# Kernel tuning notes

Measured on AMD Instinct MI355X. Metric: run time of the kernel, lower is better.

## Reference

```python
import jax, jax.numpy as jnp
import numpy as np

NUM_GRAPHS = 64
NODE_SZ = 200
FEAT = 200
HID = 256          # hidden_size; each signed branch outputs HID//2
HALF = HID // 2
N_NODES = NUM_GRAPHS * NODE_SZ
N_EDGES = 409600
NUM_LAYERS = 3


def _lin_init(key, out_f, in_f):
    kw, kb = jax.random.split(key)
    s = 1.0 / np.sqrt(in_f)
    W = jax.random.uniform(kw, (out_f, in_f), minval=-s, maxval=s, dtype=jnp.float32)
    b = jax.random.uniform(kb, (out_f,), minval=-s, maxval=s, dtype=jnp.float32)
    return W, b


def setup_inputs() -> dict:
    key = jax.random.key(0)
    ks = jax.random.split(key, 16)
    x = jax.random.normal(ks[0], (N_NODES, FEAT), dtype=jnp.float32)
    edge_index = jax.random.randint(ks[1], (2, N_EDGES), 0, N_NODES, dtype=jnp.int64)
    edge_weight = jax.random.normal(ks[2], (N_EDGES,), dtype=jnp.float32)
    batch = jnp.repeat(jnp.arange(NUM_GRAPHS, dtype=jnp.int64), NODE_SZ)

    # signed conv layer params: layer0 in=FEAT, layers 1..: in=HID; each lin maps 2*in -> HALF
    Wp0, bp0 = _lin_init(ks[3], HALF, 2 * FEAT)
    Wn0, bn0 = _lin_init(ks[4], HALF, 2 * FEAT)
    Wp1, bp1 = _lin_init(ks[5], HALF, 2 * HID)
    Wn1, bn1 = _lin_init(ks[6], HALF, 2 * HID)
    Wp2, bp2 = _lin_init(ks[7], HALF, 2 * HID)
    Wn2, bn2 = _lin_init(ks[8], HALF, 2 * HID)
    Wr, br = _lin_init(ks[9], HID, NODE_SZ * HID)   # readout_lin
    Wl, bl = _lin_init(ks[10], 1, HID)              # final lin
    return dict(x=x, edge_index=edge_index, edge_weight=edge_weight, batch=batch,
                Wp0=Wp0, bp0=bp0, Wn0=Wn0, bn0=bn0,
                Wp1=Wp1, bp1=bp1, Wn1=Wn1, bn1=bn1,
                Wp2=Wp2, bp2=bp2, Wn2=Wn2, bn2=bn2,
                Wr=Wr, br=br, Wl=Wl, bl=bl)


def _signed_conv(x, src, dst, w, Wp, bp, Wn, bn):
    # edge-weighted signed mean aggregation, split by weight sign
    xs = x[src]                                   # [E, D] gather
    pw = jnp.where(w > 0, w, 0.0)
    nw = jnp.where(w < 0, -w, 0.0)
    agg_p = jax.ops.segment_sum(pw[:, None] * xs, dst, num_segments=N_NODES)
    agg_n = jax.ops.segment_sum(nw[:, None] * xs, dst, num_segments=N_NODES)
    deg_p = jax.ops.segment_sum((w > 0).astype(x.dtype), dst, num_segments=N_NODES)
    deg_n = jax.ops.segment_sum((w < 0).astype(x.dtype), dst, num_segments=N_NODES)
    agg_p = agg_p / jnp.maximum(deg_p, 1.0)[:, None]
    agg_n = agg_n / jnp.maximum(deg_n, 1.0)[:, None]
    hp = jnp.concatenate([agg_p, x], -1) @ Wp.T + bp
    hn = jnp.concatenate([agg_n, x], -1) @ Wn.T + bn
    return jnp.concatenate([hp, hn], -1)          # [N, HID]


def reference(x, edge_index, edge_weight, batch,
              Wp0, bp0, Wn0, bn0, Wp1, bp1, Wn1, bn1, Wp2, bp2, Wn2, bn2,
              Wr, br, Wl, bl):
    src, dst = edge_index[0], edge_index[1]
    convs = [(Wp0, bp0, Wn0, bn0), (Wp1, bp1, Wn1, bn1), (Wp2, bp2, Wn2, bn2)]
    h = x
    for i, (Wp, bp, Wn, bn) in enumerate(convs):
        h = _signed_conv(h, src, dst, edge_weight, Wp, bp, Wn, bn)
        if i < NUM_LAYERS - 1:
            h = jax.nn.leaky_relu(h, negative_slope=0.01)
    # per-graph readout: batch is contiguous with NODE_SZ nodes per graph,
    # so the boolean-mask+view loop is exactly a reshape.
    g = h.reshape(NUM_GRAPHS, NODE_SZ * HID)
    g = g @ Wr.T + br                             # [G, HID]
    # dropout(p=0.5) is identity in eval mode
    return g @ Wl.T + bl                          # [G, 1]
```

## Files before the change

### kernel.cpp

```cpp
#include <hip/hip_runtime.h>

#define NUM_GRAPHS 64
#define NODE_SZ    200
#define FEAT       200
#define HID        256
#define HALF       128
#define N_NODES    (NUM_GRAPHS * NODE_SZ)
#define KREAD      (NODE_SZ * HID)
#define KSTRIDE    512
#define HBLK       128

typedef unsigned short ushort_t;
typedef unsigned int uint_t;
typedef __attribute__((ext_vector_type(8))) short bf16x8;
typedef __attribute__((ext_vector_type(4))) float f32x4;

#define GAS(p) ((const __attribute__((address_space(1))) void*)(p))
#define LAS(p) ((__attribute__((address_space(3))) void*)(p))

__device__ __forceinline__ float bf2f(ushort_t u) {
    union { unsigned int i; float f; } v; v.i = ((unsigned int)u) << 16; return v.f;
}
__device__ __forceinline__ ushort_t f2bf(float f) {
    union { float f; unsigned int i; } v; v.f = f;
    unsigned int x = v.i;
    unsigned int r = (x + 0x7fffu + ((x >> 16) & 1u)) >> 16;
    return (ushort_t)r;
}

__global__ __launch_bounds__(1024) void bhist_kernel(const int* __restrict__ ei,
                                                     const float* __restrict__ ew,
                                                     uint_t* __restrict__ bh, int E) {
    __shared__ uint_t h[N_NODES];
    for (int i = threadIdx.x; i < N_NODES; i += 1024) h[i] = 0;
    __syncthreads();
    int b = blockIdx.x;
    int epb = (E + HBLK - 1) / HBLK;
    int e0 = b * epb, e1 = min(e0 + epb, E);
    for (int e = e0 + threadIdx.x; e < e1; e += 1024) {
        int dst = ei[E + e];
        float w = ew[e];
        if (w > 0.0f)      atomicAdd(&h[dst], 1u);
        else if (w < 0.0f) atomicAdd(&h[dst], 0x10000u);
    }
    __syncthreads();
    uint_t* out = bh + (size_t)b * N_NODES;
    for (int i = threadIdx.x * 4; i < N_NODES; i += 4096)
        *(uint4*)&out[i] = *(const uint4*)&h[i];
}

__global__ void colpref_kernel(uint_t* __restrict__ bh, int* __restrict__ counts,
                               int* __restrict__ cnt_p) {
    int n = blockIdx.x * 256 + threadIdx.x;
    if (n >= N_NODES) return;
    uint_t seq = 0;
    for (int b = 0; b < HBLK; ++b) {
        size_t i = (size_t)b * N_NODES + n;
        uint_t v = bh[i];
        bh[i] = seq;
        seq += v;
    }
    counts[n] = (int)((seq & 0xffffu) + (seq >> 16));
    cnt_p[n]  = (int)(seq & 0xffffu);
}

__global__ __launch_bounds__(1024) void scan_kernel(const int* __restrict__ counts,
                                                    const int* __restrict__ cnt_p,
                                                    uint2* __restrict__ obnd, int n) {
    const int PER = 13;
    int t = threadIdx.x;
    int start = t * PER;
    int local[PER];
    int sum = 0;
#pragma unroll
    for (int i = 0; i < PER; ++i) {
        int idx = start + i;
        int v = (idx < n) ? counts[idx] : 0;
        local[i] = sum;
        sum += v;
    }
    int lane = t & 63, wid = t >> 6;
    int inc = sum;
#pragma unroll
    for (int d = 1; d < 64; d <<= 1) {
        int up = __shfl_up(inc, d);
        if (lane >= d) inc += up;
    }
    __shared__ int wsum[16], woff[16];
    if (lane == 63) wsum[wid] = inc;
    __syncthreads();
    if (t < 16) {
        int acc = 0;
        for (int j = 0; j < 16; ++j) if (j < t) acc += wsum[j];
        woff[t] = acc;
    }
    __syncthreads();
    int base = woff[wid] + (inc - sum);
#pragma unroll
    for (int i = 0; i < PER; ++i) {
        int idx = start + i;
        if (idx < n) {
            uint_t off = (uint_t)(base + local[i]);
            obnd[idx] = make_uint2(off, off + (uint_t)cnt_p[idx]);
        }
    }
    if (t == 1023) {
        uint_t tot = (uint_t)(base + sum);
        obnd[n] = make_uint2(tot, tot);
    }
}

__global__ __launch_bounds__(1024) void scat_kernel(const int* __restrict__ ei,
                                                    const float* __restrict__ ew,
                                                    const uint_t* __restrict__ bh,
                                                    const uint2* __restrict__ obnd,
                                                    uint2* __restrict__ es, int E) {
    __shared__ uint_t cur[N_NODES];
    int b = blockIdx.x;
    const uint_t* pref = bh + (size_t)b * N_NODES;
    for (int i = threadIdx.x * 4; i < N_NODES; i += 4096)
        *(uint4*)&cur[i] = *(const uint4*)&pref[i];
    __syncthreads();
    int epb = (E + HBLK - 1) / HBLK;
    int e0 = b * epb, e1 = min(e0 + epb, E);
    for (int e = e0 + threadIdx.x; e < e1; e += 1024) {
        int src = ei[e];
        int dst = ei[E + e];
        float w = ew[e];
        if (w > 0.0f) {
            uint_t old = atomicAdd(&cur[dst], 1u);
            uint_t pos = obnd[dst].x + (old & 0xffffu);
            es[pos] = make_uint2((uint_t)src, __float_as_uint(w));
        } else if (w < 0.0f) {
            uint_t old = atomicAdd(&cur[dst], 0x10000u);
            uint_t pos = obnd[dst].y + (old >> 16);
            es[pos] = make_uint2((uint_t)src, __float_as_uint(-w));
        }
    }
}

__global__ void prep_kernel(const float* __restrict__ W0p, const float* __restrict__ W0n,
                            const float* __restrict__ W1p, const float* __restrict__ W1n,
                            const float* __restrict__ W2p, const float* __restrict__ W2n,
                            const float* __restrict__ x,
                            ushort_t* __restrict__ wcast, ushort_t* __restrict__ xb) {
    int task = blockIdx.y;
    if (task < 6) {
        if (blockIdx.x >= 256) return;
        const float* W = (task == 0) ? W0p : (task == 1) ? W0n : (task == 2) ? W1p
                       : (task == 3) ? W1n : (task == 4) ? W2p : W2n;
        int K2 = (task < 2) ? 400 : 512;
        int idx = blockIdx.x * 256 + threadIdx.x;
        int row = idx >> 9;
        int col = idx & (KSTRIDE - 1);
        wcast[task * 65536 + idx] = (col < K2) ? f2bf(W[(size_t)row * K2 + col]) : (ushort_t)0;
    } else {
        int i = (blockIdx.x * 256 + threadIdx.x) * 4;
        if (i >= N_NODES * FEAT) return;
        float4 v = *(const float4*)&x[i];
        ushort4 o;
        o.x = f2bf(v.x); o.y = f2bf(v.y); o.z = f2bf(v.z); o.w = f2bf(v.w);
        *(ushort4*)&xb[i] = o;
    }
}

template <int D>
__global__ __launch_bounds__(256) void agg_kernel(
        const ushort_t* __restrict__ hb,
        const uint2* __restrict__ obnd,
        const uint2* __restrict__ es,
        ushort_t* __restrict__ Ap, ushort_t* __restrict__ An) {
    constexpr int ACT = D / 4;
    int lane = threadIdx.x & 63;
    int wv   = threadIdx.x >> 6;
    int n = blockIdx.x * 4 + wv;
    int c0 = min(lane, ACT - 1) * 4;
    uint2 ob = obnd[n];
    uint_t off = ob.x, mid = ob.y, end = obnd[n + 1].x;

    float ap[4] = {0.f, 0.f, 0.f, 0.f};
    float an[4] = {0.f, 0.f, 0.f, 0.f};

#pragma unroll 1
    for (int phase = 0; phase < 2; ++phase) {
        uint_t lo = phase ? mid : off;
        uint_t hi = phase ? end : mid;
        float* acc = phase ? an : ap;
#pragma unroll 1
        for (uint_t base = lo; base < hi; base += 64) {
            int cnt = (int)min(64u, hi - base);
            uint2 rec = es[base + (uint_t)min(lane, cnt - 1)];
            int i = 0;
#pragma unroll 1
            for (; i + 8 <= cnt; i += 8) {
                int s[8]; float w[8]; uint2 p[8];
#pragma unroll
                for (int j = 0; j < 8; ++j) {
                    s[j] = __shfl((int)rec.x, i + j);
                    w[j] = __uint_as_float((uint_t)__shfl((int)rec.y, i + j));
                }
#pragma unroll
                for (int j = 0; j < 8; ++j) p[j] = *(const uint2*)&hb[(size_t)s[j] * D + c0];
#pragma unroll
                for (int j = 0; j < 8; ++j) {
                    const ushort_t* q = (const ushort_t*)&p[j];
#pragma unroll
                    for (int c = 0; c < 4; ++c) acc[c] = fmaf(w[j], bf2f(q[c]), acc[c]);
                }
            }
#pragma unroll 1
            for (; i < cnt; ++i) {
                int s = __shfl((int)rec.x, i);
                float w = __uint_as_float((uint_t)__shfl((int)rec.y, i));
                uint2 pk = *(const uint2*)&hb[(size_t)s * D + c0];
                const ushort_t* q = (const ushort_t*)&pk;
#pragma unroll
                for (int c = 0; c < 4; ++c) acc[c] = fmaf(w, bf2f(q[c]), acc[c]);
            }
        }
    }

    size_t rb = (size_t)n * KSTRIDE;
    if (lane < ACT) {
        float dp = fmaxf((float)(mid - off), 1.0f);
        float dn = fmaxf((float)(end - mid), 1.0f);
        uint2 pk = *(const uint2*)&hb[(size_t)n * D + c0];
        const ushort_t* p = (const ushort_t*)&pk;
        ushort4 os = {p[0], p[1], p[2], p[3]};
        ushort4 op, on;
        op.x = f2bf(ap[0] / dp); op.y = f2bf(ap[1] / dp);
        op.z = f2bf(ap[2] / dp); op.w = f2bf(ap[3] / dp);
        on.x = f2bf(an[0] / dn); on.y = f2bf(an[1] / dn);
        on.z = f2bf(an[2] / dn); on.w = f2bf(an[3] / dn);
        *(ushort4*)&Ap[rb + c0] = op;
        *(ushort4*)&An[rb + c0] = on;
        *(ushort4*)&Ap[rb + D + c0] = os;
        *(ushort4*)&An[rb + D + c0] = os;
    }
    if (D == 200 && lane >= 50 && lane < 54) {
        ushort4 z = {0, 0, 0, 0};
        *(ushort4*)&Ap[rb + 400 + (lane - 50) * 4] = z;
        *(ushort4*)&An[rb + 400 + (lane - 50) * 4] = z;
    }
}

template <int KSTEPS, bool LEAKY>
__global__ __launch_bounds__(256) void conv_mfma(
        const ushort_t* __restrict__ Ap, const ushort_t* __restrict__ An,
        const ushort_t* __restrict__ Wpb, const ushort_t* __restrict__ Wnb,
        const float* __restrict__ bp, const float* __restrict__ bn,
        ushort_t* __restrict__ hout) {
    __shared__ __align__(16) ushort_t As[2][64 * 32];
    __shared__ __align__(16) ushort_t Bs[2][128 * 32];
    int mBase = blockIdx.x * 64;
    bool neg = (blockIdx.y != 0);
    const ushort_t* A    = neg ? An : Ap;
    const ushort_t* W    = neg ? Wnb : Wpb;
    const float*    bias = neg ? bn : bp;
    int tid  = threadIdx.x;
    int lane = tid & 63;
    int wv   = tid >> 6;
    int r    = lane & 15;
    int quad = lane >> 4;

    int rowA = tid >> 2, colA = (tid & 3) * 8;
    const ushort_t* gA  = A + (size_t)(mBase + rowA) * KSTRIDE + colA;
    const ushort_t* gB0 = W + (size_t)rowA * KSTRIDE + colA;
    const ushort_t* gB1 = W + (size_t)(rowA + 64) * KSTRIDE + colA;

    f32x4 acc[8];
#pragma unroll
    for (int j = 0; j < 8; ++j) acc[j] = (f32x4){0.f, 0.f, 0.f, 0.f};

    __builtin_amdgcn_global_load_lds(GAS(gA),  LAS(&As[0][wv * 512]), 16, 0, 0);
    __builtin_amdgcn_global_load_lds(GAS(gB0), LAS(&Bs[0][wv * 512]), 16, 0, 0);
    __builtin_amdgcn_global_load_lds(GAS(gB1), LAS(&Bs[0][2048 + wv * 512]), 16, 0, 0);

    for (int kt = 0; kt < KSTEPS; ++kt) {
        int cur = kt & 1;
        __syncthreads();
        if (kt + 1 < KSTEPS) {
            int kB = (kt + 1) * 32;
            __builtin_amdgcn_global_load_lds(GAS(gA + kB),  LAS(&As[cur ^ 1][wv * 512]), 16, 0, 0);
            __builtin_amdgcn_global_load_lds(GAS(gB0 + kB), LAS(&Bs[cur ^ 1][wv * 512]), 16, 0, 0);
            __builtin_amdgcn_global_load_lds(GAS(gB1 + kB), LAS(&Bs[cur ^ 1][2048 + wv * 512]), 16, 0, 0);
        }
        bf16x8 a = *(const bf16x8*)&As[cur][(wv * 16 + r) * 32 + quad * 8];
#pragma unroll
        for (int j = 0; j < 8; ++j) {
            bf16x8 b = *(const bf16x8*)&Bs[cur][(j * 16 + r) * 32 + quad * 8];
            acc[j] = __builtin_amdgcn_mfma_f32_16x16x32_bf16(a, b, acc[j], 0, 0, 0);
        }
    }
    int colOff = neg ? HALF : 0;
#pragma unroll
    for (int j = 0; j < 8; ++j) {
        int c = j * 16 + r;
        float bv = bias[c];
#pragma unroll
        for (int reg = 0; reg < 4; ++reg) {
            int m = mBase + wv * 16 + quad * 4 + reg;
            float v = acc[j][reg] + bv;
            if (LEAKY) v = (v > 0.0f) ? v : 0.01f * v;
            hout[(size_t)m * HID + colOff + c] = f2bf(v);
        }
    }
}

__global__ __launch_bounds__(256) void readout_mfma(
        const ushort_t* __restrict__ h, const float* __restrict__ Wr,
        float* __restrict__ g_ws) {
    __shared__ __align__(16) ushort_t As[64 * 32];
    __shared__ __align__(16) ushort_t Bs[64 * 32];
    int nBase  = blockIdx.x * 64;
    int kStart = blockIdx.y * 800;
    int tid  = threadIdx.x;
    int lane = tid & 63;
    int wv   = tid >> 6;
    int r    = lane & 15;
    int quad = lane >> 4;

    f32x4 acc[4];
#pragma unroll
    for (int j = 0; j < 4; ++j) acc[j] = (f32x4){0.f, 0.f, 0.f, 0.f};

    for (int kt = 0; kt < 25; ++kt) {
        int kBase = kStart + kt * 32;
        int lin = tid * 8;
        int row = lin >> 5, col = lin & 31;
        *(uint4*)&As[lin] = *(const uint4*)&h[(size_t)row * KREAD + kBase + col];
        {
            const float* wp = &Wr[(size_t)(nBase + row) * KREAD + kBase + col];
            float4 f0 = *(const float4*)&wp[0];
            float4 f1 = *(const float4*)&wp[4];
            ushort4 b0, b1;
            b0.x = f2bf(f0.x); b0.y = f2bf(f0.y); b0.z = f2bf(f0.z); b0.w = f2bf(f0.w);
            b1.x = f2bf(f1.x); b1.y = f2bf(f1.y); b1.z = f2bf(f1.z); b1.w = f2bf(f1.w);
            *(ushort4*)&Bs[lin]     = b0;
            *(ushort4*)&Bs[lin + 4] = b1;
        }
        __syncthreads();
        bf16x8 a = *(const bf16x8*)&As[(wv * 16 + r) * 32 + quad * 8];
#pragma unroll
        for (int j = 0; j < 4; ++j) {
            bf16x8 b = *(const bf16x8*)&Bs[(j * 16 + r) * 32 + quad * 8];
            acc[j] = __builtin_amdgcn_mfma_f32_16x16x32_bf16(a, b, acc[j], 0, 0, 0);
        }
        __syncthreads();
    }
#pragma unroll
    for (int j = 0; j < 4; ++j) {
        int c = nBase + j * 16 + r;
#pragma unroll
        for (int reg = 0; reg < 4; ++reg) {
            int g = wv * 16 + quad * 4 + reg;
            atomicAdd(&g_ws[g * HID + c], acc[j][reg]);
        }
    }
}

__global__ void final_kernel(const float* __restrict__ g_ws, const float* __restrict__ br,
                             const float* __restrict__ Wl, const float* __restrict__ bl,
                             float* __restrict__ out) {
    int g = blockIdx.x;
    int c = threadIdx.x;
    float v = (g_ws[g * HID + c] + br[c]) * Wl[c];
#pragma unroll
    for (int d = 32; d > 0; d >>= 1) v += __shfl_down(v, d);
    __shared__ float s[4];
    if ((c & 63) == 0) s[c >> 6] = v;
    __syncthreads();
    if (c == 0) out[g] = s[0] + s[1] + s[2] + s[3] + bl[0];
}

extern "C" void kernel_launch(void* const* d_in, const int* in_sizes, int n_in,
                              void* d_out, int out_size, void* d_ws, size_t ws_size,
                              hipStream_t stream) {
    const float* x  = (const float*)d_in[0];
    const int*   ei = (const int*)d_in[1];
    const float* ew = (const float*)d_in[2];
    const float* Wp0 = (const float*)d_in[4];
    const float* bp0 = (const float*)d_in[5];
    const float* Wn0 = (const float*)d_in[6];
    const float* bn0 = (const float*)d_in[7];
    const float* Wp1 = (const float*)d_in[8];
    const float* bp1 = (const float*)d_in[9];
    const float* Wn1 = (const float*)d_in[10];
    const float* bn1 = (const float*)d_in[11];
    const float* Wp2 = (const float*)d_in[12];
    const float* bp2 = (const float*)d_in[13];
    const float* Wn2 = (const float*)d_in[14];
    const float* bn2 = (const float*)d_in[15];
    const float* Wr  = (const float*)d_in[16];
    const float* br  = (const float*)d_in[17];
    const float* Wl  = (const float*)d_in[18];
    const float* bl  = (const float*)d_in[19];
    const int E = in_sizes[1] / 2;

    char* ws = (char*)d_ws;
    float*    g_ws   = (float*)(ws + 0);
    uint_t*   bh     = (uint_t*)(ws + 65536);
    int*      counts = (int*)(ws + 6619136);
    int*      cnt_p  = (int*)(ws + 6670336);
    uint2*    obnd   = (uint2*)(ws + 6721536);
    uint2*    es     = (uint2*)(ws + 6824000);
    ushort_t* Ap     = (ushort_t*)(ws + 10100800);
    ushort_t* An     = (ushort_t*)(ws + 23208000);
    ushort_t* hA     = (ushort_t*)(ws + 36315200);
    ushort_t* hB     = (ushort_t*)(ws + 42868800);
    ushort_t* wcast  = (ushort_t*)(ws + 49422400);
    ushort_t* xb     = (ushort_t*)(ws + 50208832);

    ushort_t* w0p = wcast + 0 * 65536;
    ushort_t* w0n = wcast + 1 * 65536;
    ushort_t* w1p = wcast + 2 * 65536;
    ushort_t* w1n = wcast + 3 * 65536;
    ushort_t* w2p = wcast + 4 * 65536;
    ushort_t* w2n = wcast + 5 * 65536;

    hipMemsetAsync(g_ws, 0, 65536, stream);

    hipLaunchKernelGGL(bhist_kernel, dim3(HBLK), dim3(1024), 0, stream, ei, ew, bh, E);
    hipLaunchKernelGGL(colpref_kernel, dim3((N_NODES + 255) / 256), dim3(256), 0, stream,
                       bh, counts, cnt_p);
    hipLaunchKernelGGL(scan_kernel, dim3(1), dim3(1024), 0, stream, counts, cnt_p, obnd, N_NODES);
    hipLaunchKernelGGL(scat_kernel, dim3(HBLK), dim3(1024), 0, stream, ei, ew, bh, obnd, es, E);

    hipLaunchKernelGGL(prep_kernel, dim3(2500, 7), dim3(256), 0, stream,
                       Wp0, Wn0, Wp1, Wn1, Wp2, Wn2, x, wcast, xb);

    hipLaunchKernelGGL((agg_kernel<FEAT>), dim3(N_NODES / 4), dim3(256), 0, stream,
                       xb, obnd, es, Ap, An);
    hipLaunchKernelGGL((conv_mfma<13, true>), dim3(N_NODES / 64, 2), dim3(256), 0, stream,
                       Ap, An, w0p, w0n, bp0, bn0, hA);
    hipLaunchKernelGGL((agg_kernel<HID>), dim3(N_NODES / 4), dim3(256), 0, stream,
                       hA, obnd, es, Ap, An);
    hipLaunchKernelGGL((conv_mfma<16, true>), dim3(N_NODES / 64, 2), dim3(256), 0, stream,
                       Ap, An, w1p, w1n, bp1, bn1, hB);
    hipLaunchKernelGGL((agg_kernel<HID>), dim3(N_NODES / 4), dim3(256), 0, stream,
                       hB, obnd, es, Ap, An);
    hipLaunchKernelGGL((conv_mfma<16, false>), dim3(N_NODES / 64, 2), dim3(256), 0, stream,
                       Ap, An, w2p, w2n, bp2, bn2, hA);

    hipLaunchKernelGGL(readout_mfma, dim3(4, 64), dim3(256), 0, stream, hA, Wr, g_ws);
    hipLaunchKernelGGL(final_kernel, dim3(NUM_GRAPHS), dim3(256), 0, stream,
                       g_ws, br, Wl, bl, (float*)d_out);
}
```

Baseline: 315.2 us.

## Fuse signed aggregation with per-layer MFMA linear into one kernel

Each conv layer now runs as a single kernel: a 32-node block gathers the positive and negative neighbour sums into an LDS tile (padded stride) and immediately multiplies it by the branch weight via MFMA, writing the activated output. This removes the Ap/An global intermediate buffers (write plus re-read of about 13 MB per layer) and three kernel launches. In exchange, each block does 8 serial gathers per wave per branch before any MFMA work, with less parallelism (400 blocks) and no overlap between gather and matmul. The weight tiles are also reloaded per block.

Result: slower. 390.5 us (+23.9%).

```diff
diff --git a/kernel.cpp b/kernel.cpp
--- a/kernel.cpp
+++ b/kernel.cpp
@@ -8,6 +8,7 @@
 #define N_NODES    (NUM_GRAPHS * NODE_SZ)
 #define KREAD      (NODE_SZ * HID)
 #define KSTRIDE    512
+#define ASTRIDE    544
 #define HBLK       128
 
 typedef unsigned short ushort_t;
@@ -165,144 +166,144 @@
 }
 
 template <int D>
-__global__ __launch_bounds__(256) void agg_kernel(
+__device__ __forceinline__ void gather_bucket(const ushort_t* __restrict__ hb,
+                                              const uint2* __restrict__ es,
+                                              uint_t lo, uint_t hi, int c0, int lane,
+                                              float acc[4]) {
+#pragma unroll 1
+    for (uint_t base = lo; base < hi; base += 64) {
+        int cnt = (int)min(64u, hi - base);
+        uint2 rec = es[base + (uint_t)min(lane, cnt - 1)];
+        int i = 0;
+#pragma unroll 1
+        for (; i + 8 <= cnt; i += 8) {
+            int s[8]; float w[8]; uint2 p[8];
+#pragma unroll
+            for (int j = 0; j < 8; ++j) {
+                s[j] = __shfl((int)rec.x, i + j);
+                w[j] = __uint_as_float((uint_t)__shfl((int)rec.y, i + j));
+            }
+#pragma unroll
+            for (int j = 0; j < 8; ++j) p[j] = *(const uint2*)&hb[(size_t)s[j] * D + c0];
+#pragma unroll
+            for (int j = 0; j < 8; ++j) {
+                const ushort_t* q = (const ushort_t*)&p[j];
+#pragma unroll
+                for (int c = 0; c < 4; ++c) acc[c] = fmaf(w[j], bf2f(q[c]), acc[c]);
+            }
+        }
+#pragma unroll 1
+        for (; i < cnt; ++i) {
+            int s = __shfl((int)rec.x, i);
+            float w = __uint_as_float((uint_t)__shfl((int)rec.y, i));
+            uint2 pk = *(const uint2*)&hb[(size_t)s * D + c0];
+            const ushort_t* q = (const ushort_t*)&pk;
+#pragma unroll
+            for (int c = 0; c < 4; ++c) acc[c] = fmaf(w, bf2f(q[c]), acc[c]);
+        }
+    }
+}
+
+template <int D, int KSTEPS, bool LEAKY>
+__global__ __launch_bounds__(256) void fused_layer(
         const ushort_t* __restrict__ hb,
-        const uint2* __restrict__ obnd,
-        const uint2* __restrict__ es,
-        ushort_t* __restrict__ Ap, ushort_t* __restrict__ An) {
-    constexpr int ACT = D / 4;
-    int lane = threadIdx.x & 63;
-    int wv   = threadIdx.x >> 6;
-    int n = blockIdx.x * 4 + wv;
-    int c0 = min(lane, ACT - 1) * 4;
-    uint2 ob = obnd[n];
-    uint_t off = ob.x, mid = ob.y, end = obnd[n + 1].x;
-
-    float ap[4] = {0.f, 0.f, 0.f, 0.f};
-    float an[4] = {0.f, 0.f, 0.f, 0.f};
-
-#pragma unroll 1
-    for (int phase = 0; phase < 2; ++phase) {
-        uint_t lo = phase ? mid : off;
-        uint_t hi = phase ? end : mid;
-        float* acc = phase ? an : ap;
-#pragma unroll 1
-        for (uint_t base = lo; base < hi; base += 64) {
-            int cnt = (int)min(64u, hi - base);
-            uint2 rec = es[base + (uint_t)min(lane, cnt - 1)];
-            int i = 0;
-#pragma unroll 1
-            for (; i + 8 <= cnt; i += 8) {
-                int s[8]; float w[8]; uint2 p[8];
-#pragma unroll
-                for (int j = 0; j < 8; ++j) {
-                    s[j] = __shfl((int)rec.x, i + j);
-                    w[j] = __uint_as_float((uint_t)__shfl((int)rec.y, i + j));
-                }
-#pragma unroll
-                for (int j = 0; j < 8; ++j) p[j] = *(const uint2*)&hb[(size_t)s[j] * D + c0];
-#pragma unroll
-                for (int j = 0; j < 8; ++j) {
-                    const ushort_t* q = (const ushort_t*)&p[j];
-#pragma unroll
-                    for (int c = 0; c < 4; ++c) acc[c] = fmaf(w[j], bf2f(q[c]), acc[c]);
-                }
-            }
-#pragma unroll 1
-            for (; i < cnt; ++i) {
-                int s = __shfl((int)rec.x, i);
-                float w = __uint_as_float((uint_t)__shfl((int)rec.y, i));
-                uint2 pk = *(const uint2*)&hb[(size_t)s * D + c0];
-                const ushort_t* q = (const ushort_t*)&pk;
-#pragma unroll
-                for (int c = 0; c < 4; ++c) acc[c] = fmaf(w, bf2f(q[c]), acc[c]);
-            }
-        }
-    }
-
-    size_t rb = (size_t)n * KSTRIDE;
-    if (lane < ACT) {
-        float dp = fmaxf((float)(mid - off), 1.0f);
-        float dn = fmaxf((float)(end - mid), 1.0f);
-        uint2 pk = *(const uint2*)&hb[(size_t)n * D + c0];
-        const ushort_t* p = (const ushort_t*)&pk;
-        ushort4 os = {p[0], p[1], p[2], p[3]};
-        ushort4 op, on;
-        op.x = f2bf(ap[0] / dp); op.y = f2bf(ap[1] / dp);
-        op.z = f2bf(ap[2] / dp); op.w = f2bf(ap[3] / dp);
-        on.x = f2bf(an[0] / dn); on.y = f2bf(an[1] / dn);
-        on.z = f2bf(an[2] / dn); on.w = f2bf(an[3] / dn);
-        *(ushort4*)&Ap[rb + c0] = op;
-        *(ushort4*)&An[rb + c0] = on;
-        *(ushort4*)&Ap[rb + D + c0] = os;
-        *(ushort4*)&An[rb + D + c0] = os;
-    }
-    if (D == 200 && lane >= 50 && lane < 54) {
-        ushort4 z = {0, 0, 0, 0};
-        *(ushort4*)&Ap[rb + 400 + (lane - 50) * 4] = z;
-        *(ushort4*)&An[rb + 400 + (lane - 50) * 4] = z;
-    }
-}
-
-template <int KSTEPS, bool LEAKY>
-__global__ __launch_bounds__(256) void conv_mfma(
-        const ushort_t* __restrict__ Ap, const ushort_t* __restrict__ An,
+        const uint2* __restrict__ obnd, const uint2* __restrict__ es,
         const ushort_t* __restrict__ Wpb, const ushort_t* __restrict__ Wnb,
         const float* __restrict__ bp, const float* __restrict__ bn,
         ushort_t* __restrict__ hout) {
-    __shared__ __align__(16) ushort_t As[2][64 * 32];
+    __shared__ __align__(16) ushort_t At[32 * ASTRIDE];
     __shared__ __align__(16) ushort_t Bs[2][128 * 32];
-    int mBase = blockIdx.x * 64;
-    bool neg = (blockIdx.y != 0);
-    const ushort_t* A    = neg ? An : Ap;
-    const ushort_t* W    = neg ? Wnb : Wpb;
-    const float*    bias = neg ? bn : bp;
+    constexpr int ACT = D / 4;
     int tid  = threadIdx.x;
     int lane = tid & 63;
     int wv   = tid >> 6;
     int r    = lane & 15;
     int quad = lane >> 4;
-
-    int rowA = tid >> 2, colA = (tid & 3) * 8;
-    const ushort_t* gA  = A + (size_t)(mBase + rowA) * KSTRIDE + colA;
-    const ushort_t* gB0 = W + (size_t)rowA * KSTRIDE + colA;
-    const ushort_t* gB1 = W + (size_t)(rowA + 64) * KSTRIDE + colA;
-
-    f32x4 acc[8];
-#pragma unroll
-    for (int j = 0; j < 8; ++j) acc[j] = (f32x4){0.f, 0.f, 0.f, 0.f};
-
-    __builtin_amdgcn_global_load_lds(GAS(gA),  LAS(&As[0][wv * 512]), 16, 0, 0);
-    __builtin_amdgcn_global_load_lds(GAS(gB0), LAS(&Bs[0][wv * 512]), 16, 0, 0);
-    __builtin_amdgcn_global_load_lds(GAS(gB1), LAS(&Bs[0][2048 + wv * 512]), 16, 0, 0);
-
-    for (int kt = 0; kt < KSTEPS; ++kt) {
-        int cur = kt & 1;
+    int nBase = blockIdx.x * 32;
+    int c0 = min(lane, ACT - 1) * 4;
+
+    int rowB = tid >> 2, colB = (tid & 3) * 8;
+
+#pragma unroll 1
+    for (int branch = 0; branch < 2; ++branch) {
+        const ushort_t* W    = branch ? Wnb : Wpb;
+        const float*    bias = branch ? bn : bp;
+#pragma unroll 1
+        for (int i = 0; i < 8; ++i) {
+            int nloc = wv * 8 + i;
+            int n = nBase + nloc;
+            uint2 ob = obnd[n];
+            uint_t nx = obnd[n + 1].x;
+            uint_t lo = branch ? ob.y : ob.x;
+            uint_t hi = branch ? nx : ob.y;
+            float acc[4] = {0.f, 0.f, 0.f, 0.f};
+            gather_bucket<D>(hb, es, lo, hi, c0, lane, acc);
+            float deg = fmaxf((float)(hi - lo), 1.0f);
+            if (lane < ACT) {
+                ushort4 oa;
+                oa.x = f2bf(acc[0] / deg); oa.y = f2bf(acc[1] / deg);
+                oa.z = f2bf(acc[2] / deg); oa.w = f2bf(acc[3] / deg);
+                *(ushort4*)&At[nloc * ASTRIDE + c0] = oa;
+                if (branch == 0) {
+                    uint2 pk = *(const uint2*)&hb[(size_t)n * D + c0];
+                    const ushort_t* p = (const ushort_t*)&pk;
+                    ushort4 os = {p[0], p[1], p[2], p[3]};
+                    *(ushort4*)&At[nloc * ASTRIDE + D + c0] = os;
+                }
+            }
+            if (branch == 0 && D == 200 && lane >= 50 && lane < 54) {
+                ushort4 z = {0, 0, 0, 0};
+                *(ushort4*)&At[nloc * ASTRIDE + 400 + (lane - 50) * 4] = z;
+            }
+        }
+        const ushort_t* gB0 = W + (size_t)rowB * KSTRIDE + colB;
+        const ushort_t* gB1 = W + (size_t)(rowB + 64) * KSTRIDE + colB;
+        __builtin_amdgcn_global_load_lds(GAS(gB0), LAS(&Bs[0][wv * 512]), 16, 0, 0);
+        __builtin_amdgcn_global_load_lds(GAS(gB1), LAS(&Bs[0][2048 + wv * 512]), 16, 0, 0);
         __syncthreads();
-        if (kt + 1 < KSTEPS) {
-            int kB = (kt + 1) * 32;
-            __builtin_amdgcn_global_load_lds(GAS(gA + kB),  LAS(&As[cur ^ 1][wv * 512]), 16, 0, 0);
-            __builtin_amdgcn_global_load_lds(GAS(gB0 + kB), LAS(&Bs[cur ^ 1][wv * 512]), 16, 0, 0);
-            __builtin_amdgcn_global_load_lds(GAS(gB1 + kB), LAS(&Bs[cur ^ 1][2048 + wv * 512]), 16, 0, 0);
-        }
-        bf16x8 a = *(const bf16x8*)&As[cur][(wv * 16 + r) * 32 + quad * 8];
-#pragma unroll
-        for (int j = 0; j < 8; ++j) {
-            bf16x8 b = *(const bf16x8*)&Bs[cur][(j * 16 + r) * 32 + quad * 8];
-            acc[j] = __builtin_amdgcn_mfma_f32_16x16x32_bf16(a, b, acc[j], 0, 0, 0);
-        }
-    }
-    int colOff = neg ? HALF : 0;
-#pragma unroll
-    for (int j = 0; j < 8; ++j) {
-        int c = j * 16 + r;
-        float bv = bias[c];
-#pragma unroll
-        for (int reg = 0; reg < 4; ++reg) {
-            int m = mBase + wv * 16 + quad * 4 + reg;
-            float v = acc[j][reg] + bv;
-            if (LEAKY) v = (v > 0.0f) ? v : 0.01f * v;
-            hout[(size_t)m * HID + colOff + c] = f2bf(v);
+
+        f32x4 acc00 = {0.f,0.f,0.f,0.f}, acc01 = {0.f,0.f,0.f,0.f};
+        f32x4 acc10 = {0.f,0.f,0.f,0.f}, acc11 = {0.f,0.f,0.f,0.f};
+#pragma unroll 1
+        for (int kt = 0; kt < KSTEPS; ++kt) {
+            int cur = kt & 1;
+            if (kt > 0) __syncthreads();
+            if (kt + 1 < KSTEPS) {
+                int kB = (kt + 1) * 32;
+                __builtin_amdgcn_global_load_lds(GAS(gB0 + kB), LAS(&Bs[cur ^ 1][wv * 512]), 16, 0, 0);
+                __builtin_amdgcn_global_load_lds(GAS(gB1 + kB), LAS(&Bs[cur ^ 1][2048 + wv * 512]), 16, 0, 0);
+            }
+            bf16x8 a0 = *(const bf16x8*)&At[r * ASTRIDE + kt * 32 + quad * 8];
+            bf16x8 a1 = *(const bf16x8*)&At[(16 + r) * ASTRIDE + kt * 32 + quad * 8];
+            bf16x8 b0 = *(const bf16x8*)&Bs[cur][(wv * 32 + r) * 32 + quad * 8];
+            bf16x8 b1 = *(const bf16x8*)&Bs[cur][(wv * 32 + 16 + r) * 32 + quad * 8];
+            acc00 = __builtin_amdgcn_mfma_f32_16x16x32_bf16(a0, b0, acc00, 0, 0, 0);
+            acc01 = __builtin_amdgcn_mfma_f32_16x16x32_bf16(a0, b1, acc01, 0, 0, 0);
+            acc10 = __builtin_amdgcn_mfma_f32_16x16x32_bf16(a1, b0, acc10, 0, 0, 0);
+            acc11 = __builtin_amdgcn_mfma_f32_16x16x32_bf16(a1, b1, acc11, 0, 0, 0);
+        }
+        __syncthreads();
+
+        int colOff = branch * HALF + wv * 32;
+#pragma unroll
+        for (int jn = 0; jn < 2; ++jn) {
+            int cl = wv * 32 + jn * 16 + r;
+            float bv = bias[cl];
+            f32x4 am0 = jn ? acc01 : acc00;
+            f32x4 am1 = jn ? acc11 : acc10;
+#pragma unroll
+            for (int reg = 0; reg < 4; ++reg) {
+                int m0 = nBase + quad * 4 + reg;
+                int m1 = m0 + 16;
+                float v0 = am0[reg] + bv;
+                float v1 = am1[reg] + bv;
+                if (LEAKY) {
+                    v0 = (v0 > 0.0f) ? v0 : 0.01f * v0;
+                    v1 = (v1 > 0.0f) ? v1 : 0.01f * v1;
+                }
+                hout[(size_t)m0 * HID + colOff + jn * 16 + r] = f2bf(v0);
+                hout[(size_t)m1 * HID + colOff + jn * 16 + r] = f2bf(v1);
+            }
         }
     }
 }
@@ -404,8 +405,6 @@
     int*      cnt_p  = (int*)(ws + 6670336);
     uint2*    obnd   = (uint2*)(ws + 6721536);
     uint2*    es     = (uint2*)(ws + 6824000);
-    ushort_t* Ap     = (ushort_t*)(ws + 10100800);
-    ushort_t* An     = (ushort_t*)(ws + 23208000);
     ushort_t* hA     = (ushort_t*)(ws + 36315200);
     ushort_t* hB     = (ushort_t*)(ws + 42868800);
     ushort_t* wcast  = (ushort_t*)(ws + 49422400);
@@ -429,18 +428,12 @@
     hipLaunchKernelGGL(prep_kernel, dim3(2500, 7), dim3(256), 0, stream,
                        Wp0, Wn0, Wp1, Wn1, Wp2, Wn2, x, wcast, xb);
 
-    hipLaunchKernelGGL((agg_kernel<FEAT>), dim3(N_NODES / 4), dim3(256), 0, stream,
-                       xb, obnd, es, Ap, An);
-    hipLaunchKernelGGL((conv_mfma<13, true>), dim3(N_NODES / 64, 2), dim3(256), 0, stream,
-                       Ap, An, w0p, w0n, bp0, bn0, hA);
-    hipLaunchKernelGGL((agg_kernel<HID>), dim3(N_NODES / 4), dim3(256), 0, stream,
-                       hA, obnd, es, Ap, An);
-    hipLaunchKernelGGL((conv_mfma<16, true>), dim3(N_NODES / 64, 2), dim3(256), 0, stream,
-                       Ap, An, w1p, w1n, bp1, bn1, hB);
-    hipLaunchKernelGGL((agg_kernel<HID>), dim3(N_NODES / 4), dim3(256), 0, stream,
-                       hB, obnd, es, Ap, An);
-    hipLaunchKernelGGL((conv_mfma<16, false>), dim3(N_NODES / 64, 2), dim3(256), 0, stream,
-                       Ap, An, w2p, w2n, bp2, bn2, hA);
+    hipLaunchKernelGGL((fused_layer<FEAT, 13, true>), dim3(N_NODES / 32), dim3(256), 0, stream,
+                       xb, obnd, es, w0p, w0n, bp0, bn0, hA);
+    hipLaunchKernelGGL((fused_layer<HID, 16, true>), dim3(N_NODES / 32), dim3(256), 0, stream,
+                       hA, obnd, es, w1p, w1n, bp1, bn1, hB);
+    hipLaunchKernelGGL((fused_layer<HID, 16, false>), dim3(N_NODES / 32), dim3(256), 0, stream,
+                       hB, obnd, es, w2p, w2n, bp2, bn2, hA);
 
     hipLaunchKernelGGL(readout_mfma, dim3(4, 64), dim3(256), 0, stream, hA, Wr, g_ws);
     hipLaunchKernelGGL(final_kernel, dim3(NUM_GRAPHS), dim3(256), 0, stream,
```

## Parallelize column prefix with wave scans and deepen gather unroll in aggregation

Applied to the files above, without the earlier changes.

The per-node column prefix over 128 histogram blocks used to run as a serial loop, one thread per node. It now uses one wavefront per node with two 64-lane shuffle-based inclusive scans. The aggregation inner loop now issues 16 gathers per batch instead of 8, and a 4-wide tail loop is added, to expose more memory-level parallelism. The trade-off is that the colpref loads become strided across lanes, so they are uncoalesced, and the wider unroll raises register pressure.

After: 328.9 us. 1.04x slower.

```diff
diff --git a/kernel.cpp b/kernel.cpp
--- a/kernel.cpp
+++ b/kernel.cpp
@@ -49,19 +49,29 @@
         *(uint4*)&out[i] = *(const uint4*)&h[i];
 }
 
-__global__ void colpref_kernel(uint_t* __restrict__ bh, int* __restrict__ counts,
-                               int* __restrict__ cnt_p) {
-    int n = blockIdx.x * 256 + threadIdx.x;
-    if (n >= N_NODES) return;
-    uint_t seq = 0;
-    for (int b = 0; b < HBLK; ++b) {
-        size_t i = (size_t)b * N_NODES + n;
-        uint_t v = bh[i];
-        bh[i] = seq;
-        seq += v;
-    }
-    counts[n] = (int)((seq & 0xffffu) + (seq >> 16));
-    cnt_p[n]  = (int)(seq & 0xffffu);
+__global__ __launch_bounds__(256) void colpref_kernel(uint_t* __restrict__ bh,
+                                                      int* __restrict__ counts,
+                                                      int* __restrict__ cnt_p) {
+    int lane = threadIdx.x & 63, wv = threadIdx.x >> 6;
+    int n = blockIdx.x * 4 + wv;
+    size_t i0 = (size_t)lane * N_NODES + n;
+    size_t i1 = (size_t)(lane + 64) * N_NODES + n;
+    uint_t v0 = bh[i0], v1 = bh[i1];
+    uint_t s0 = v0, s1 = v1;
+#pragma unroll
+    for (int d = 1; d < 64; d <<= 1) {
+        uint_t u0 = (uint_t)__shfl_up((int)s0, d);
+        uint_t u1 = (uint_t)__shfl_up((int)s1, d);
+        if (lane >= d) { s0 += u0; s1 += u1; }
+    }
+    uint_t tot0 = (uint_t)__shfl((int)s0, 63);
+    bh[i0] = s0 - v0;
+    bh[i1] = tot0 + s1 - v1;
+    if (lane == 63) {
+        uint_t tot = tot0 + s1;
+        counts[n] = (int)((tot & 0xffffu) + (tot >> 16));
+        cnt_p[n]  = (int)(tot & 0xffffu);
+    }
 }
 
 __global__ __launch_bounds__(1024) void scan_kernel(const int* __restrict__ counts,
@@ -192,17 +202,34 @@
             uint2 rec = es[base + (uint_t)min(lane, cnt - 1)];
             int i = 0;
 #pragma unroll 1
-            for (; i + 8 <= cnt; i += 8) {
-                int s[8]; float w[8]; uint2 p[8];
-#pragma unroll
-                for (int j = 0; j < 8; ++j) {
+            for (; i + 16 <= cnt; i += 16) {
+                int s[16]; float w[16]; uint2 p[16];
+#pragma unroll
+                for (int j = 0; j < 16; ++j) {
                     s[j] = __shfl((int)rec.x, i + j);
                     w[j] = __uint_as_float((uint_t)__shfl((int)rec.y, i + j));
                 }
 #pragma unroll
-                for (int j = 0; j < 8; ++j) p[j] = *(const uint2*)&hb[(size_t)s[j] * D + c0];
-#pragma unroll
-                for (int j = 0; j < 8; ++j) {
+                for (int j = 0; j < 16; ++j) p[j] = *(const uint2*)&hb[(size_t)s[j] * D + c0];
+#pragma unroll
+                for (int j = 0; j < 16; ++j) {
+                    const ushort_t* q = (const ushort_t*)&p[j];
+#pragma unroll
+                    for (int c = 0; c < 4; ++c) acc[c] = fmaf(w[j], bf2f(q[c]), acc[c]);
+                }
+            }
+#pragma unroll 1
+            for (; i + 4 <= cnt; i += 4) {
+                int s[4]; float w[4]; uint2 p[4];
+#pragma unroll
+                for (int j = 0; j < 4; ++j) {
+                    s[j] = __shfl((int)rec.x, i + j);
+                    w[j] = __uint_as_float((uint_t)__shfl((int)rec.y, i + j));
+                }
+#pragma unroll
+                for (int j = 0; j < 4; ++j) p[j] = *(const uint2*)&hb[(size_t)s[j] * D + c0];
+#pragma unroll
+                for (int j = 0; j < 4; ++j) {
                     const ushort_t* q = (const ushort_t*)&p[j];
 #pragma unroll
                     for (int c = 0; c < 4; ++c) acc[c] = fmaf(w[j], bf2f(q[c]), acc[c]);
@@ -421,7 +448,7 @@
     hipMemsetAsync(g_ws, 0, 65536, stream);
 
     hipLaunchKernelGGL(bhist_kernel, dim3(HBLK), dim3(1024), 0, stream, ei, ew, bh, E);
-    hipLaunchKernelGGL(colpref_kernel, dim3((N_NODES + 255) / 256), dim3(256), 0, stream,
+    hipLaunchKernelGGL(colpref_kernel, dim3(N_NODES / 4), dim3(256), 0, stream,
                        bh, counts, cnt_p);
     hipLaunchKernelGGL(scan_kernel, dim3(1), dim3(1024), 0, stream, counts, cnt_p, obnd, N_NODES);
     hipLaunchKernelGGL(scat_kernel, dim3(HBLK), dim3(1024), 0, stream, ei, ew, bh, obnd, es, E);
```
